# Performance work log

Measured on AMD Instinct MI355X. Metric: run time of the kernel, lower is better.

The kernel has to match this reference:

```python
import jax, jax.numpy as jnp
import numpy as np

EMBED_DIM = 256
HIDDEN_DIM = 128
NUM_VARS = 1024


def _linear_params(key, fan_in, fan_out):
    kw, kb = jax.random.split(key)
    lim = 1.0 / np.sqrt(fan_in)
    W = jax.random.uniform(kw, (fan_in, fan_out), minval=-lim, maxval=lim, dtype=jnp.float32)
    b = jax.random.uniform(kb, (fan_out,), minval=-lim, maxval=lim, dtype=jnp.float32)
    return W, b


def setup_inputs() -> dict:
    key = jax.random.key(0)
    ks = jax.random.split(key, 7)
    next_state_embedding = jax.random.normal(ks[0], (EMBED_DIM,), dtype=jnp.float32)
    prev_variable_embeddings = jax.random.normal(ks[1], (NUM_VARS, EMBED_DIM), dtype=jnp.float32)
    Wq, bq = _linear_params(ks[2], EMBED_DIM, HIDDEN_DIM)
    Wk, bk = _linear_params(ks[3], EMBED_DIM, HIDDEN_DIM)
    Wc, bc = _linear_params(ks[4], EMBED_DIM, HIDDEN_DIM)
    W1, b1 = _linear_params(ks[5], 2 * HIDDEN_DIM, HIDDEN_DIM)
    W2, b2 = _linear_params(ks[6], HIDDEN_DIM, 1)
    return {
        "next_state_embedding": next_state_embedding,
        "prev_variable_embeddings": prev_variable_embeddings,
        "Wq": Wq, "bq": bq,
        "Wk": Wk, "bk": bk,
        "Wc": Wc, "bc": bc,
        "W1": W1, "b1": b1,
        "W2": W2, "b2": b2,
    }


def reference(next_state_embedding, prev_variable_embeddings,
              Wq, bq, Wk, bk, Wc, bc, W1, b1, W2, b2):
    n = prev_variable_embeddings.shape[0]
    h = Wq.shape[1]
    # context_net: Linear + ReLU on next-state embedding -> [h]
    context = jax.nn.relu(next_state_embedding @ Wc + bc)
    # queries/keys over prev vars, each shifted by context -> [n, h]
    queries = prev_variable_embeddings @ Wq + bq + context
    keys = prev_variable_embeddings @ Wk + bk + context
    # pair_scorer layer 1 on concat(q_i, k_j) decomposes:
    # hidden[i,j] = relu(q_i @ W1[:h] + k_j @ W1[h:] + b1)
    q_proj = queries @ W1[:h]            # [n, h]
    k_proj = keys @ W1[h:]               # [n, h]
    hidden = jax.nn.relu(q_proj[:, None, :] + k_proj[None, :, :] + b1)  # [n, n, h]
    scores = jnp.squeeze(hidden @ W2, axis=-1) + b2[0]  # [n, n]
    # extract i < j pairs in row-major order (matches the nested loop)
    iu, ju = jnp.triu_indices(n, k=1)
    return scores[iu, ju]  # [n*(n-1)/2]
```

## Files before the change

kernel.cpp:

```cpp
#include <hip/hip_runtime.h>

#define N 1024
#define E 256
#define H 128

typedef _Float16 hv2 __attribute__((ext_vector_type(2)));
typedef _Float16 half_t;

__device__ __forceinline__ float dot2_acc(hv2 a, hv2 b, float c) {
#if __has_builtin(__builtin_amdgcn_fdot2)
    return __builtin_amdgcn_fdot2(a, b, c, false);
#else
    return c + (float)a.x * (float)b.x + (float)a.y * (float)b.y;
#endif
}

__device__ __forceinline__ hv2 relu_add2(hv2 a, hv2 b) {
    hv2 s = a + b;
    hv2 z = (hv2)(_Float16)0.f;
    return __builtin_elementwise_max(s, z);
}

__global__ __launch_bounds__(256) void setup_kernel(
    const float* __restrict__ x, const float* __restrict__ Wc, const float* __restrict__ bc,
    const float* __restrict__ Wq, const float* __restrict__ bq,
    const float* __restrict__ Wk, const float* __restrict__ bk,
    const float* __restrict__ W1, const float* __restrict__ b1,
    float* __restrict__ Wqp, float* __restrict__ Wkp,
    float* __restrict__ constq, float* __restrict__ constk) {
    int b = blockIdx.x;
    int t = threadIdx.x;
    if (b < E) {
        __shared__ float wq_s[H], wk_s[H];
        if (t < H) wq_s[t] = Wq[b * H + t];
        else       wk_s[t - H] = Wk[b * H + (t - H)];
        __syncthreads();
        int h = t & (H - 1);
        float acc = 0.f;
        if (t < H) {
#pragma unroll 8
            for (int r = 0; r < H; ++r) acc += wq_s[r] * W1[r * H + h];
            Wqp[b * H + h] = acc;
        } else {
#pragma unroll 8
            for (int r = 0; r < H; ++r) acc += wk_s[r] * W1[(H + r) * H + h];
            Wkp[b * H + h] = acc;
        }
    } else {
        __shared__ float xs[E];
        __shared__ float pc[2][H];
        __shared__ float aq_s[H], ak_s[H];
        xs[t] = x[t];
        __syncthreads();
        int h = t & (H - 1);
        int c = t >> 7;
        float p = 0.f;
#pragma unroll 8
        for (int e = c * H; e < c * H + H; ++e) p += xs[e] * Wc[e * H + h];
        pc[c][h] = p;
        __syncthreads();
        if (t < H) {
            float ctxv = fmaxf(pc[0][t] + pc[1][t] + bc[t], 0.f);
            aq_s[t] = bq[t] + ctxv;
            ak_s[t] = bk[t] + ctxv;
        }
        __syncthreads();
        float acc;
        if (t < H) {
            acc = b1[h];
#pragma unroll 8
            for (int r = 0; r < H; ++r) acc += aq_s[r] * W1[r * H + h];
            constq[h] = acc;
        } else {
            acc = 0.f;
#pragma unroll 8
            for (int r = 0; r < H; ++r) acc += ak_s[r] * W1[(H + r) * H + h];
            constk[h] = acc;
        }
    }
}

__global__ __launch_bounds__(256) void proj_kernel(
    const float* __restrict__ P,
    const float* __restrict__ Wqp, const float* __restrict__ Wkp,
    const float* __restrict__ constq, const float* __restrict__ constk,
    half_t* __restrict__ qh, half_t* __restrict__ kh) {
    __shared__ __align__(16) float p_s[2 * E];
    int b = blockIdx.x;
    int i0 = b * 2;
    int t = threadIdx.x;
    if (t < 128) ((float4*)p_s)[t] = ((const float4*)(P + i0 * E))[t];
    __syncthreads();
    bool isq = t < H;
    int h = t & (H - 1);
    const float* M = isq ? Wqp : Wkp;
    float cv = isq ? constq[h] : constk[h];
    float a0 = cv, a1 = cv;
    for (int e = 0; e < E; e += 8) {
        float m0 = M[(e + 0) * H + h];
        float m1 = M[(e + 1) * H + h];
        float m2 = M[(e + 2) * H + h];
        float m3 = M[(e + 3) * H + h];
        float m4 = M[(e + 4) * H + h];
        float m5 = M[(e + 5) * H + h];
        float m6 = M[(e + 6) * H + h];
        float m7 = M[(e + 7) * H + h];
        float4 p0a = *(const float4*)&p_s[0 * E + e];
        float4 p0b = *(const float4*)&p_s[0 * E + e + 4];
        float4 p1a = *(const float4*)&p_s[1 * E + e];
        float4 p1b = *(const float4*)&p_s[1 * E + e + 4];
        a0 += p0a.x * m0 + p0a.y * m1 + p0a.z * m2 + p0a.w * m3
            + p0b.x * m4 + p0b.y * m5 + p0b.z * m6 + p0b.w * m7;
        a1 += p1a.x * m0 + p1a.y * m1 + p1a.z * m2 + p1a.w * m3
            + p1b.x * m4 + p1b.y * m5 + p1b.z * m6 + p1b.w * m7;
    }
    half_t* O = isq ? qh : kh;
    O[(i0 + 0) * H + h] = (half_t)a0;
    O[(i0 + 1) * H + h] = (half_t)a1;
}

#define QSTR 136
#define NTILE 32
__global__ __launch_bounds__(256) void pair_kernel(
    const half_t* __restrict__ qh, const half_t* __restrict__ kh,
    const float* __restrict__ W2, const float* __restrict__ b2,
    float* __restrict__ out) {
    int tid = blockIdx.x;
    int bi = (int)((65.0f - sqrtf(4225.0f - 8.0f * (float)tid)) * 0.5f);
    while (bi > 0 && tid < 32 * bi - bi * (bi - 1) / 2) --bi;
    while (tid >= 32 * (bi + 1) - (bi + 1) * bi / 2) ++bi;
    int bj = bi + (tid - (32 * bi - bi * (bi - 1) / 2));

    __shared__ __align__(16) half_t qs[32][QSTR];
    __shared__ __align__(16) half_t ks[32][QSTR];
    __shared__ __align__(16) half_t w2s[H];

    int t = threadIdx.x;
    if (t < H) w2s[t] = (half_t)W2[t];

    const float4* qh4 = (const float4*)(qh + bi * 32 * H);
    const float4* kh4 = (const float4*)(kh + bj * 32 * H);
#pragma unroll
    for (int v = 0; v < 2; ++v) {
        int idx = v * 256 + t;
        int r = idx >> 4, c = idx & 15;
        float4 q = qh4[idx];
        float4 k = kh4[idx];
        *(float4*)&qs[r][c * 8] = q;
        *(float4*)&ks[r][c * 8] = k;
    }
    __syncthreads();

    int jj  = t & 31;
    int ti0 = t >> 5;
    float b2v = b2[0];
    float acc[4];
#pragma unroll
    for (int u = 0; u < 4; ++u) acc[u] = b2v;

    for (int h8 = 0; h8 < 16; ++h8) {
        float4 wf = *(const float4*)&w2s[h8 * 8];
        float4 kv = *(const float4*)&ks[jj][h8 * 8];
        const hv2* wp = (const hv2*)&wf;
        const hv2* kp2 = (const hv2*)&kv;
#pragma unroll
        for (int u = 0; u < 4; ++u) {
            float4 qf = *(const float4*)&qs[ti0 + u * 8][h8 * 8];
            const hv2* qp2 = (const hv2*)&qf;
#pragma unroll
            for (int s = 0; s < 4; ++s) {
                hv2 sa = relu_add2(qp2[s], kp2[s]);
                acc[u] = dot2_acc(sa, wp[s], acc[u]);
            }
        }
    }

#pragma unroll
    for (int u = 0; u < 4; ++u) {
        int i = bi * 32 + ti0 + u * 8;
        int j = bj * 32 + jj;
        if (j > i) {
            int base = i * (2 * N - i - 1) / 2;
            out[base + (j - i - 1)] = acc[u];
        }
    }
}

extern "C" void kernel_launch(void* const* d_in, const int* in_sizes, int n_in,
                              void* d_out, int out_size, void* d_ws, size_t ws_size,
                              hipStream_t stream) {
    const float* x  = (const float*)d_in[0];
    const float* P  = (const float*)d_in[1];
    const float* Wq = (const float*)d_in[2];
    const float* bq = (const float*)d_in[3];
    const float* Wk = (const float*)d_in[4];
    const float* bk = (const float*)d_in[5];
    const float* Wc = (const float*)d_in[6];
    const float* bc = (const float*)d_in[7];
    const float* W1 = (const float*)d_in[8];
    const float* b1 = (const float*)d_in[9];
    const float* W2 = (const float*)d_in[10];
    const float* b2 = (const float*)d_in[11];
    float* out = (float*)d_out;

    float* ws     = (float*)d_ws;
    float* constq = ws;
    float* constk = ws + H;
    float* Wqp    = ws + 2 * H;
    float* Wkp    = Wqp + E * H;
    half_t* qh    = (half_t*)(Wkp + E * H);
    half_t* kh    = qh + N * H;

    setup_kernel<<<E + 1, 256, 0, stream>>>(x, Wc, bc, Wq, bq, Wk, bk, W1, b1,
                                            Wqp, Wkp, constq, constk);
    proj_kernel<<<N / 2, 256, 0, stream>>>(P, Wqp, Wkp, constq, constk, qh, kh);
    pair_kernel<<<528, 256, 0, stream>>>(qh, kh, W2, b2, out);
}
```

Baseline: 101.4 us.

## Fuse setup, projection and pair kernels into one cooperative kernel with grid syncs

Merges the three separate launches into a single cooperative kernel of 528 blocks, using grid-wide syncs between the weight-folding, projection and pair-scoring phases. Shared memory is reused across phases through one aliased buffer. The aim is to remove two kernel launches and their inter-kernel gaps. In exchange it adds two grid barriers and cooperative launch overhead, and 528 blocks must all be co-resident on the GPU.

```diff
diff --git a/kernel.cpp b/kernel.cpp
--- a/kernel.cpp
+++ b/kernel.cpp
@@ -1,8 +1,12 @@
 #include <hip/hip_runtime.h>
+#include <hip/hip_cooperative_groups.h>
+
+namespace cg = cooperative_groups;
 
 #define N 1024
 #define E 256
 #define H 128
+#define QSTR 136
 
 typedef _Float16 hv2 __attribute__((ext_vector_type(2)));
 typedef _Float16 half_t;
@@ -21,17 +25,30 @@
     return __builtin_elementwise_max(s, z);
 }
 
-__global__ __launch_bounds__(256) void setup_kernel(
-    const float* __restrict__ x, const float* __restrict__ Wc, const float* __restrict__ bc,
+__global__ __launch_bounds__(256, 3) void fused_kernel(
+    const float* __restrict__ x, const float* __restrict__ P,
     const float* __restrict__ Wq, const float* __restrict__ bq,
     const float* __restrict__ Wk, const float* __restrict__ bk,
+    const float* __restrict__ Wc, const float* __restrict__ bc,
     const float* __restrict__ W1, const float* __restrict__ b1,
+    const float* __restrict__ W2, const float* __restrict__ b2,
     float* __restrict__ Wqp, float* __restrict__ Wkp,
-    float* __restrict__ constq, float* __restrict__ constk) {
+    float* __restrict__ constq, float* __restrict__ constk,
+    half_t* __restrict__ qh, half_t* __restrict__ kh,
+    float* __restrict__ out) {
+    cg::grid_group grid = cg::this_grid();
+
+    __shared__ __align__(16) half_t qs[32][QSTR];
+    __shared__ __align__(16) half_t ks[32][QSTR];
+    __shared__ __align__(16) half_t w2s[H];
+    float* fs = (float*)&qs[0][0];
+
     int b = blockIdx.x;
     int t = threadIdx.x;
+
     if (b < E) {
-        __shared__ float wq_s[H], wk_s[H];
+        float* wq_s = fs;
+        float* wk_s = fs + H;
         if (t < H) wq_s[t] = Wq[b * H + t];
         else       wk_s[t - H] = Wk[b * H + (t - H)];
         __syncthreads();
@@ -46,10 +63,11 @@
             for (int r = 0; r < H; ++r) acc += wk_s[r] * W1[(H + r) * H + h];
             Wkp[b * H + h] = acc;
         }
-    } else {
-        __shared__ float xs[E];
-        __shared__ float pc[2][H];
-        __shared__ float aq_s[H], ak_s[H];
+    } else if (b == E) {
+        float* xs   = fs;
+        float* pc   = fs + E;
+        float* aq_s = fs + E + 2 * H;
+        float* ak_s = fs + E + 3 * H;
         xs[t] = x[t];
         __syncthreads();
         int h = t & (H - 1);
@@ -57,131 +75,118 @@
         float p = 0.f;
 #pragma unroll 8
         for (int e = c * H; e < c * H + H; ++e) p += xs[e] * Wc[e * H + h];
-        pc[c][h] = p;
+        pc[c * H + h] = p;
         __syncthreads();
         if (t < H) {
-            float ctxv = fmaxf(pc[0][t] + pc[1][t] + bc[t], 0.f);
+            float ctxv = fmaxf(pc[t] + pc[H + t] + bc[t], 0.f);
             aq_s[t] = bq[t] + ctxv;
             ak_s[t] = bk[t] + ctxv;
         }
         __syncthreads();
-        float acc;
         if (t < H) {
-            acc = b1[h];
+            float acc = b1[h];
 #pragma unroll 8
             for (int r = 0; r < H; ++r) acc += aq_s[r] * W1[r * H + h];
             constq[h] = acc;
         } else {
-            acc = 0.f;
+            float acc = 0.f;
 #pragma unroll 8
             for (int r = 0; r < H; ++r) acc += ak_s[r] * W1[(H + r) * H + h];
             constk[h] = acc;
         }
     }
-}
-
-__global__ __launch_bounds__(256) void proj_kernel(
-    const float* __restrict__ P,
-    const float* __restrict__ Wqp, const float* __restrict__ Wkp,
-    const float* __restrict__ constq, const float* __restrict__ constk,
-    half_t* __restrict__ qh, half_t* __restrict__ kh) {
-    __shared__ __align__(16) float p_s[2 * E];
-    int b = blockIdx.x;
-    int i0 = b * 2;
-    int t = threadIdx.x;
-    if (t < 128) ((float4*)p_s)[t] = ((const float4*)(P + i0 * E))[t];
-    __syncthreads();
-    bool isq = t < H;
-    int h = t & (H - 1);
-    const float* M = isq ? Wqp : Wkp;
-    float cv = isq ? constq[h] : constk[h];
-    float a0 = cv, a1 = cv;
-    for (int e = 0; e < E; e += 8) {
-        float m0 = M[(e + 0) * H + h];
-        float m1 = M[(e + 1) * H + h];
-        float m2 = M[(e + 2) * H + h];
-        float m3 = M[(e + 3) * H + h];
-        float m4 = M[(e + 4) * H + h];
-        float m5 = M[(e + 5) * H + h];
-        float m6 = M[(e + 6) * H + h];
-        float m7 = M[(e + 7) * H + h];
-        float4 p0a = *(const float4*)&p_s[0 * E + e];
-        float4 p0b = *(const float4*)&p_s[0 * E + e + 4];
-        float4 p1a = *(const float4*)&p_s[1 * E + e];
-        float4 p1b = *(const float4*)&p_s[1 * E + e + 4];
-        a0 += p0a.x * m0 + p0a.y * m1 + p0a.z * m2 + p0a.w * m3
-            + p0b.x * m4 + p0b.y * m5 + p0b.z * m6 + p0b.w * m7;
-        a1 += p1a.x * m0 + p1a.y * m1 + p1a.z * m2 + p1a.w * m3
-            + p1b.x * m4 + p1b.y * m5 + p1b.z * m6 + p1b.w * m7;
+
+    grid.sync();
+
+    if (b < N / 2) {
+        float* p_s = fs;
+        int i0 = b * 2;
+        if (t < 128) ((float4*)p_s)[t] = ((const float4*)(P + i0 * E))[t];
+        __syncthreads();
+        bool isq = t < H;
+        int h = t & (H - 1);
+        const float* M = isq ? Wqp : Wkp;
+        float cv = isq ? constq[h] : constk[h];
+        float a0 = cv, a1 = cv;
+        for (int e = 0; e < E; e += 8) {
+            float m0 = M[(e + 0) * H + h];
+            float m1 = M[(e + 1) * H + h];
+            float m2 = M[(e + 2) * H + h];
+            float m3 = M[(e + 3) * H + h];
+            float m4 = M[(e + 4) * H + h];
+            float m5 = M[(e + 5) * H + h];
+            float m6 = M[(e + 6) * H + h];
+            float m7 = M[(e + 7) * H + h];
+            float4 p0a = *(const float4*)&p_s[0 * E + e];
+            float4 p0b = *(const float4*)&p_s[0 * E + e + 4];
+            float4 p1a = *(const float4*)&p_s[1 * E + e];
+            float4 p1b = *(const float4*)&p_s[1 * E + e + 4];
+            a0 += p0a.x * m0 + p0a.y * m1 + p0a.z * m2 + p0a.w * m3
+                + p0b.x * m4 + p0b.y * m5 + p0b.z * m6 + p0b.w * m7;
+            a1 += p1a.x * m0 + p1a.y * m1 + p1a.z * m2 + p1a.w * m3
+                + p1b.x * m4 + p1b.y * m5 + p1b.z * m6 + p1b.w * m7;
+        }
+        half_t* O = isq ? qh : kh;
+        O[(i0 + 0) * H + h] = (half_t)a0;
+        O[(i0 + 1) * H + h] = (half_t)a1;
     }
-    half_t* O = isq ? qh : kh;
-    O[(i0 + 0) * H + h] = (half_t)a0;
-    O[(i0 + 1) * H + h] = (half_t)a1;
-}
-
-#define QSTR 136
-#define NTILE 32
-__global__ __launch_bounds__(256) void pair_kernel(
-    const half_t* __restrict__ qh, const half_t* __restrict__ kh,
-    const float* __restrict__ W2, const float* __restrict__ b2,
-    float* __restrict__ out) {
-    int tid = blockIdx.x;
-    int bi = (int)((65.0f - sqrtf(4225.0f - 8.0f * (float)tid)) * 0.5f);
-    while (bi > 0 && tid < 32 * bi - bi * (bi - 1) / 2) --bi;
-    while (tid >= 32 * (bi + 1) - (bi + 1) * bi / 2) ++bi;
-    int bj = bi + (tid - (32 * bi - bi * (bi - 1) / 2));
-
-    __shared__ __align__(16) half_t qs[32][QSTR];
-    __shared__ __align__(16) half_t ks[32][QSTR];
-    __shared__ __align__(16) half_t w2s[H];
-
-    int t = threadIdx.x;
-    if (t < H) w2s[t] = (half_t)W2[t];
-
-    const float4* qh4 = (const float4*)(qh + bi * 32 * H);
-    const float4* kh4 = (const float4*)(kh + bj * 32 * H);
-#pragma unroll
-    for (int v = 0; v < 2; ++v) {
-        int idx = v * 256 + t;
-        int r = idx >> 4, c = idx & 15;
-        float4 q = qh4[idx];
-        float4 k = kh4[idx];
-        *(float4*)&qs[r][c * 8] = q;
-        *(float4*)&ks[r][c * 8] = k;
-    }
-    __syncthreads();
-
-    int jj  = t & 31;
-    int ti0 = t >> 5;
-    float b2v = b2[0];
-    float acc[4];
-#pragma unroll
-    for (int u = 0; u < 4; ++u) acc[u] = b2v;
-
-    for (int h8 = 0; h8 < 16; ++h8) {
-        float4 wf = *(const float4*)&w2s[h8 * 8];
-        float4 kv = *(const float4*)&ks[jj][h8 * 8];
-        const hv2* wp = (const hv2*)&wf;
-        const hv2* kp2 = (const hv2*)&kv;
+
+    grid.sync();
+
+    {
+        int tid = b;
+        int bi = (int)((65.0f - sqrtf(4225.0f - 8.0f * (float)tid)) * 0.5f);
+        while (bi > 0 && tid < 32 * bi - bi * (bi - 1) / 2) --bi;
+        while (tid >= 32 * (bi + 1) - (bi + 1) * bi / 2) ++bi;
+        int bj = bi + (tid - (32 * bi - bi * (bi - 1) / 2));
+
+        if (t < H) w2s[t] = (half_t)W2[t];
+
+        const float4* qh4 = (const float4*)(qh + bi * 32 * H);
+        const float4* kh4 = (const float4*)(kh + bj * 32 * H);
+#pragma unroll
+        for (int v = 0; v < 2; ++v) {
+            int idx = v * 256 + t;
+            int r = idx >> 4, c = idx & 15;
+            float4 q = qh4[idx];
+            float4 k = kh4[idx];
+            *(float4*)&qs[r][c * 8] = q;
+            *(float4*)&ks[r][c * 8] = k;
+        }
+        __syncthreads();
+
+        int jj  = t & 31;
+        int ti0 = t >> 5;
+        float b2v = b2[0];
+        float acc[4];
+#pragma unroll
+        for (int u = 0; u < 4; ++u) acc[u] = b2v;
+
+        for (int h8 = 0; h8 < 16; ++h8) {
+            float4 wf = *(const float4*)&w2s[h8 * 8];
+            float4 kv = *(const float4*)&ks[jj][h8 * 8];
+            const hv2* wp = (const hv2*)&wf;
+            const hv2* kp2 = (const hv2*)&kv;
+#pragma unroll
+            for (int u = 0; u < 4; ++u) {
+                float4 qf = *(const float4*)&qs[ti0 + u * 8][h8 * 8];
+                const hv2* qp2 = (const hv2*)&qf;
+#pragma unroll
+                for (int s = 0; s < 4; ++s) {
+                    hv2 sa = relu_add2(qp2[s], kp2[s]);
+                    acc[u] = dot2_acc(sa, wp[s], acc[u]);
+                }
+            }
+        }
+
 #pragma unroll
         for (int u = 0; u < 4; ++u) {
-            float4 qf = *(const float4*)&qs[ti0 + u * 8][h8 * 8];
-            const hv2* qp2 = (const hv2*)&qf;
-#pragma unroll
-            for (int s = 0; s < 4; ++s) {
-                hv2 sa = relu_add2(qp2[s], kp2[s]);
-                acc[u] = dot2_acc(sa, wp[s], acc[u]);
+            int i = bi * 32 + ti0 + u * 8;
+            int j = bj * 32 + jj;
+            if (j > i) {
+                int base = i * (2 * N - i - 1) / 2;
+                out[base + (j - i - 1)] = acc[u];
             }
-        }
-    }
-
-#pragma unroll
-    for (int u = 0; u < 4; ++u) {
-        int i = bi * 32 + ti0 + u * 8;
-        int j = bj * 32 + jj;
-        if (j > i) {
-            int base = i * (2 * N - i - 1) / 2;
-            out[base + (j - i - 1)] = acc[u];
         }
     }
 }
@@ -211,8 +216,11 @@
     half_t* qh    = (half_t*)(Wkp + E * H);
     half_t* kh    = qh + N * H;
 
-    setup_kernel<<<E + 1, 256, 0, stream>>>(x, Wc, bc, Wq, bq, Wk, bk, W1, b1,
-                                            Wqp, Wkp, constq, constk);
-    proj_kernel<<<N / 2, 256, 0, stream>>>(P, Wqp, Wkp, constq, constk, qh, kh);
-    pair_kernel<<<528, 256, 0, stream>>>(qh, kh, W2, b2, out);
-}
+    void* args[] = {
+        (void*)&x,  (void*)&P,  (void*)&Wq, (void*)&bq, (void*)&Wk, (void*)&bk,
+        (void*)&Wc, (void*)&bc, (void*)&W1, (void*)&b1, (void*)&W2, (void*)&b2,
+        (void*)&Wqp, (void*)&Wkp, (void*)&constq, (void*)&constk,
+        (void*)&qh, (void*)&kh, (void*)&out};
+    hipLaunchCooperativeKernel((const void*)fused_kernel, dim3(528), dim3(256),
+                               args, 0, stream);
+}
```

Result: slower. 222.8 us (+119.7%).

## Fuse setup into projection kernel and drop precomputed weight products

Applied to the files above, without the earlier changes.

Removes the separate setup kernel that precomputed Wq·W1a, Wk·W1b and the context constants. Each projection block now computes the context itself, projects its two rows through Wq/Wk, and then through W1 halves using shared memory. This saves one kernel launch and its serialization, but every one of the 512 blocks redundantly recomputes the context matvec and does an extra H×H matvec per row.

```diff
diff --git a/kernel.cpp b/kernel.cpp
--- a/kernel.cpp
+++ b/kernel.cpp
@@ -21,106 +21,95 @@
     return __builtin_elementwise_max(s, z);
 }
 
-__global__ __launch_bounds__(256) void setup_kernel(
-    const float* __restrict__ x, const float* __restrict__ Wc, const float* __restrict__ bc,
+__global__ __launch_bounds__(256) void proj_kernel(
+    const float* __restrict__ x, const float* __restrict__ P,
     const float* __restrict__ Wq, const float* __restrict__ bq,
     const float* __restrict__ Wk, const float* __restrict__ bk,
+    const float* __restrict__ Wc, const float* __restrict__ bc,
     const float* __restrict__ W1, const float* __restrict__ b1,
-    float* __restrict__ Wqp, float* __restrict__ Wkp,
-    float* __restrict__ constq, float* __restrict__ constk) {
-    int b = blockIdx.x;
-    int t = threadIdx.x;
-    if (b < E) {
-        __shared__ float wq_s[H], wk_s[H];
-        if (t < H) wq_s[t] = Wq[b * H + t];
-        else       wk_s[t - H] = Wk[b * H + (t - H)];
-        __syncthreads();
-        int h = t & (H - 1);
-        float acc = 0.f;
-        if (t < H) {
-#pragma unroll 8
-            for (int r = 0; r < H; ++r) acc += wq_s[r] * W1[r * H + h];
-            Wqp[b * H + h] = acc;
-        } else {
-#pragma unroll 8
-            for (int r = 0; r < H; ++r) acc += wk_s[r] * W1[(H + r) * H + h];
-            Wkp[b * H + h] = acc;
-        }
-    } else {
-        __shared__ float xs[E];
-        __shared__ float pc[2][H];
-        __shared__ float aq_s[H], ak_s[H];
-        xs[t] = x[t];
-        __syncthreads();
-        int h = t & (H - 1);
-        int c = t >> 7;
+    half_t* __restrict__ qh, half_t* __restrict__ kh) {
+    __shared__ __align__(16) float xs[E];
+    __shared__ __align__(16) float p_s[2 * E];
+    __shared__ float pc[2 * H];
+    __shared__ float aq[H], ak[H];
+    __shared__ float sv[2][2 * H];
+
+    int b = blockIdx.x, t = threadIdx.x;
+    int i0 = b * 2;
+    if (t < 64) ((float4*)xs)[t] = ((const float4*)x)[t];
+    else if (t < 192) ((float4*)p_s)[t - 64] = ((const float4*)(P + i0 * E))[t - 64];
+    __syncthreads();
+
+    int h = t & (H - 1);
+    int c = t >> 7;
+    {
         float p = 0.f;
 #pragma unroll 8
         for (int e = c * H; e < c * H + H; ++e) p += xs[e] * Wc[e * H + h];
-        pc[c][h] = p;
-        __syncthreads();
-        if (t < H) {
-            float ctxv = fmaxf(pc[0][t] + pc[1][t] + bc[t], 0.f);
-            aq_s[t] = bq[t] + ctxv;
-            ak_s[t] = bk[t] + ctxv;
-        }
-        __syncthreads();
-        float acc;
-        if (t < H) {
-            acc = b1[h];
-#pragma unroll 8
-            for (int r = 0; r < H; ++r) acc += aq_s[r] * W1[r * H + h];
-            constq[h] = acc;
-        } else {
-            acc = 0.f;
-#pragma unroll 8
-            for (int r = 0; r < H; ++r) acc += ak_s[r] * W1[(H + r) * H + h];
-            constk[h] = acc;
-        }
-    }
-}
-
-__global__ __launch_bounds__(256) void proj_kernel(
-    const float* __restrict__ P,
-    const float* __restrict__ Wqp, const float* __restrict__ Wkp,
-    const float* __restrict__ constq, const float* __restrict__ constk,
-    half_t* __restrict__ qh, half_t* __restrict__ kh) {
-    __shared__ __align__(16) float p_s[2 * E];
-    int b = blockIdx.x;
-    int i0 = b * 2;
-    int t = threadIdx.x;
-    if (t < 128) ((float4*)p_s)[t] = ((const float4*)(P + i0 * E))[t];
-    __syncthreads();
-    bool isq = t < H;
-    int h = t & (H - 1);
-    const float* M = isq ? Wqp : Wkp;
-    float cv = isq ? constq[h] : constk[h];
-    float a0 = cv, a1 = cv;
-    for (int e = 0; e < E; e += 8) {
-        float m0 = M[(e + 0) * H + h];
-        float m1 = M[(e + 1) * H + h];
-        float m2 = M[(e + 2) * H + h];
-        float m3 = M[(e + 3) * H + h];
-        float m4 = M[(e + 4) * H + h];
-        float m5 = M[(e + 5) * H + h];
-        float m6 = M[(e + 6) * H + h];
-        float m7 = M[(e + 7) * H + h];
-        float4 p0a = *(const float4*)&p_s[0 * E + e];
-        float4 p0b = *(const float4*)&p_s[0 * E + e + 4];
-        float4 p1a = *(const float4*)&p_s[1 * E + e];
-        float4 p1b = *(const float4*)&p_s[1 * E + e + 4];
-        a0 += p0a.x * m0 + p0a.y * m1 + p0a.z * m2 + p0a.w * m3
-            + p0b.x * m4 + p0b.y * m5 + p0b.z * m6 + p0b.w * m7;
-        a1 += p1a.x * m0 + p1a.y * m1 + p1a.z * m2 + p1a.w * m3
-            + p1b.x * m4 + p1b.y * m5 + p1b.z * m6 + p1b.w * m7;
-    }
-    half_t* O = isq ? qh : kh;
-    O[(i0 + 0) * H + h] = (half_t)a0;
-    O[(i0 + 1) * H + h] = (half_t)a1;
+        pc[c * H + h] = p;
+    }
+    __syncthreads();
+    if (t < H) {
+        float ctxv = fmaxf(pc[t] + pc[H + t] + bc[t], 0.f);
+        aq[t] = bq[t] + ctxv;
+        ak[t] = bk[t] + ctxv;
+    }
+    __syncthreads();
+
+    {
+        const float* W = c ? Wk : Wq;
+        float a0 = c ? ak[h] : aq[h];
+        float a1 = a0;
+        for (int e = 0; e < E; e += 8) {
+            float m0 = W[(e + 0) * H + h];
+            float m1 = W[(e + 1) * H + h];
+            float m2 = W[(e + 2) * H + h];
+            float m3 = W[(e + 3) * H + h];
+            float m4 = W[(e + 4) * H + h];
+            float m5 = W[(e + 5) * H + h];
+            float m6 = W[(e + 6) * H + h];
+            float m7 = W[(e + 7) * H + h];
+            float4 p0a = *(const float4*)&p_s[0 * E + e];
+            float4 p0b = *(const float4*)&p_s[0 * E + e + 4];
+            float4 p1a = *(const float4*)&p_s[1 * E + e];
+            float4 p1b = *(const float4*)&p_s[1 * E + e + 4];
+            a0 += p0a.x * m0 + p0a.y * m1 + p0a.z * m2 + p0a.w * m3
+                + p0b.x * m4 + p0b.y * m5 + p0b.z * m6 + p0b.w * m7;
+            a1 += p1a.x * m0 + p1a.y * m1 + p1a.z * m2 + p1a.w * m3
+                + p1b.x * m4 + p1b.y * m5 + p1b.z * m6 + p1b.w * m7;
+        }
+        sv[0][c * H + h] = a0;
+        sv[1][c * H + h] = a1;
+    }
+    __syncthreads();
+
+    {
+        const float* W1c = W1 + c * H * H;
+        const float* S0 = &sv[0][c * H];
+        const float* S1 = &sv[1][c * H];
+        float a0 = c ? 0.f : b1[h];
+        float a1 = a0;
+        for (int r = 0; r < H; r += 8) {
+            float w0 = W1c[(r + 0) * H + h];
+            float w1 = W1c[(r + 1) * H + h];
+            float w2 = W1c[(r + 2) * H + h];
+            float w3 = W1c[(r + 3) * H + h];
+            float w4 = W1c[(r + 4) * H + h];
+            float w5 = W1c[(r + 5) * H + h];
+            float w6 = W1c[(r + 6) * H + h];
+            float w7 = W1c[(r + 7) * H + h];
+            a0 += S0[r + 0] * w0 + S0[r + 1] * w1 + S0[r + 2] * w2 + S0[r + 3] * w3
+                + S0[r + 4] * w4 + S0[r + 5] * w5 + S0[r + 6] * w6 + S0[r + 7] * w7;
+            a1 += S1[r + 0] * w0 + S1[r + 1] * w1 + S1[r + 2] * w2 + S1[r + 3] * w3
+                + S1[r + 4] * w4 + S1[r + 5] * w5 + S1[r + 6] * w6 + S1[r + 7] * w7;
+        }
+        half_t* O = c ? kh : qh;
+        O[(i0 + 0) * H + h] = (half_t)a0;
+        O[(i0 + 1) * H + h] = (half_t)a1;
+    }
 }
 
 #define QSTR 136
-#define NTILE 32
 __global__ __launch_bounds__(256) void pair_kernel(
     const half_t* __restrict__ qh, const half_t* __restrict__ kh,
     const float* __restrict__ W2, const float* __restrict__ b2,
@@ -203,16 +192,10 @@
     const float* b2 = (const float*)d_in[11];
     float* out = (float*)d_out;
 
-    float* ws     = (float*)d_ws;
-    float* constq = ws;
-    float* constk = ws + H;
-    float* Wqp    = ws + 2 * H;
-    float* Wkp    = Wqp + E * H;
-    half_t* qh    = (half_t*)(Wkp + E * H);
-    half_t* kh    = qh + N * H;
-
-    setup_kernel<<<E + 1, 256, 0, stream>>>(x, Wc, bc, Wq, bq, Wk, bk, W1, b1,
-                                            Wqp, Wkp, constq, constk);
-    proj_kernel<<<N / 2, 256, 0, stream>>>(P, Wqp, Wkp, constq, constk, qh, kh);
+    half_t* qh = (half_t*)d_ws;
+    half_t* kh = qh + N * H;
+
+    proj_kernel<<<N / 2, 256, 0, stream>>>(x, P, Wq, bq, Wk, bk, Wc, bc, W1, b1,
+                                           qh, kh);
     pair_kernel<<<528, 256, 0, stream>>>(qh, kh, W2, b2, out);
 }
```

Result: faster. 99.27 us (-2.1%).
